# Optimization experiments

Hardware: AMD Instinct MI355X
Metric: run time of the kernel (lower is better)

The kernel has to match this reference:

```python
import jax, jax.numpy as jnp
import numpy as np

NB_KERNEL = 16
NUM_POS_EMB = 16
DMAX = 20.0


def _grbf_encode(d):
    # d: (..., ) distances; centers 0..DMAX in NB_KERNEL steps (matches torch.arange(0, 20*(1+1/15), 20/15))
    centers = jnp.linspace(0.0, DMAX, NB_KERNEL, dtype=jnp.float32)
    return jnp.exp(-jnp.square(d[..., None] - centers))


def _positional_embeddings(d):
    # d: (..., ) float offsets
    freq = jnp.exp(jnp.arange(0, NUM_POS_EMB, 2, dtype=jnp.float32) * (-(np.log(10000.0) / NUM_POS_EMB)))
    angles = d[..., None] * freq  # (..., NUM_POS_EMB//2)
    return jnp.concatenate([jnp.cos(angles), jnp.sin(angles)], axis=-1)


def setup_inputs() -> dict:
    key = jax.random.key(0)
    # coordinates in Angstrom-ish scale so pairwise distances span the RBF range
    crd = jax.random.normal(key, (4096, 4, 3), dtype=jnp.float32) * 10.0
    return {"crd": crd, "max_neigh": 64}


def reference(crd, max_neigh):
    nb_var = crd.shape[0]
    nb_neigh = min(max_neigh, nb_var - 1)

    # virtual Cbeta atom from backbone geometry
    b = crd[:, 1] - crd[:, 0]
    c = crd[:, 2] - crd[:, 1]
    a = jnp.cross(b, c)
    Cb = -0.58273431 * a + 0.56802827 * b - 0.54067466 * c + crd[:, 1]
    crd5 = jnp.concatenate([crd, Cb[:, None, :]], axis=1)  # (N, 5, 3)

    # pairwise CA distances, diagonal forced to -1 so self sorts first
    ca = crd5[:, 1]  # (N, 3)
    D = jnp.linalg.norm(ca[:, None, :] - ca[None, :, :], axis=-1)  # (N, N)
    diag = jnp.arange(nb_var)
    D = D.at[diag, diag].set(-1.0)

    # nb_neigh smallest distances (= top_k of -D); self is column 0
    neg_d, idx_pairs = jax.lax.top_k(-D, nb_neigh)  # (N, K)
    d = -neg_d
    d = d.at[:, 0].set(0.0)
    d = jnp.nan_to_num(d, nan=0.0)

    # all-pairs atom distances between residue i (5 atoms) and each neighbor j (5 atoms)
    neigh = crd5[idx_pairs]  # (N, K, 5, 3)
    diff = crd5[:, None, :, None, :] - neigh[:, :, None, :, :]  # (N, K, 5, 5, 3); [i,k,a,b]=crd[i,a]-crd[j,b]
    dist = jnp.linalg.norm(diff, axis=-1).reshape(nb_var, nb_neigh, 25)
    dist = _grbf_encode(dist).reshape(nb_var, nb_neigh, 25 * NB_KERNEL)
    dist = jnp.nan_to_num(dist, nan=0.0)

    # sinusoidal encoding of sequence-index offsets
    offsets = jnp.abs(diag[:, None] - idx_pairs).astype(jnp.float32)  # (N, K)
    pos = _positional_embeddings(offsets)  # (N, K, NUM_POS_EMB)

    return (d, dist, pos, idx_pairs)
```

## Files before the change

### kernel.cpp

```cpp
#include <hip/hip_runtime.h>
#include <math.h>

#define NBV 4096
#define KNE 64
#define D_OFF    0
#define DIST_OFF (NBV*KNE)
#define POS_OFF  (DIST_OFF + NBV*KNE*400)
#define IDX_OFF  (POS_OFF + NBV*KNE*16)

#define WS_CRD5 0
#define WS_CA4  (NBV*16)
#define WS_FLOATS (NBV*16 + NBV*4)

typedef float f4v __attribute__((ext_vector_type(4)));

__device__ __forceinline__ unsigned int f2sort(float f) {
  unsigned int u = __float_as_uint(f);
  return (u & 0x80000000u) ? ~u : (u | 0x80000000u);
}
__device__ __forceinline__ float sort2f(unsigned int s) {
  unsigned int u = (s & 0x80000000u) ? (s & 0x7FFFFFFFu) : ~s;
  return __uint_as_float(u);
}

__device__ __forceinline__ float4 crd5_f4(const float* __restrict__ crd, int r,
                                          int q) {
  if (q < 3) return ((const float4*)crd)[r * 3 + q];
  const float4 a = ((const float4*)crd)[r * 3 + 0];
  const float4 b = ((const float4*)crd)[r * 3 + 1];
  const float4 c = ((const float4*)crd)[r * 3 + 2];
  const float bx = a.w - a.x, by = b.x - a.y, bz = b.y - a.z;
  const float cx = b.z - a.w, cy = b.w - b.x, cz = c.x - b.y;
  const float axv = by * cz - bz * cy;
  const float ayv = bz * cx - bx * cz;
  const float azv = bx * cy - by * cx;
  return make_float4(
      -0.58273431f * axv + 0.56802827f * bx - 0.54067466f * cx + a.w,
      -0.58273431f * ayv + 0.56802827f * by - 0.54067466f * cy + b.x,
      -0.58273431f * azv + 0.56802827f * bz - 0.54067466f * cz + b.y, 0.0f);
}

__global__ __launch_bounds__(256) void prep_k(const float* __restrict__ crd,
                                              float* __restrict__ ws) {
  const int r = blockIdx.x * 256 + threadIdx.x;
  const float4 a = ((const float4*)crd)[r * 3 + 0];
  const float4 b = ((const float4*)crd)[r * 3 + 1];
  const float4 c = ((const float4*)crd)[r * 3 + 2];
  const float bx = a.w - a.x, by = b.x - a.y, bz = b.y - a.z;
  const float cx = b.z - a.w, cy = b.w - b.x, cz = c.x - b.y;
  const float axv = by * cz - bz * cy;
  const float ayv = bz * cx - bx * cz;
  const float azv = bx * cy - by * cx;
  const float cbx = -0.58273431f * axv + 0.56802827f * bx - 0.54067466f * cx + a.w;
  const float cby = -0.58273431f * ayv + 0.56802827f * by - 0.54067466f * cy + b.x;
  const float cbz = -0.58273431f * azv + 0.56802827f * bz - 0.54067466f * cz + b.y;

  float4* row = (float4*)(ws + WS_CRD5 + r * 16);
  row[0] = a;
  row[1] = b;
  row[2] = c;
  row[3] = make_float4(cbx, cby, cbz, 0.0f);
  ((float4*)(ws + WS_CA4))[r] = make_float4(a.w, b.x, b.y, 0.0f);
}

template <bool USE_WS>
__global__ __launch_bounds__(256) void fused_k(const float* __restrict__ crd,
                                               const float* __restrict__ ws,
                                               float* __restrict__ out) {
  const int i = blockIdx.x;
  const int t = threadIdx.x;

  __shared__ float region0[2688];
  __shared__ unsigned long long cand[512];
  __shared__ int jidx[64];
  __shared__ unsigned int cnt;
  __shared__ int selbin;
  __shared__ unsigned int wsum[4];

  unsigned int* hist = (unsigned int*)region0;
  float* rows = region0;
  float* dvals = region0 + 1040;

  for (int b = t; b < 2048; b += 256) hist[b] = 0u;
  if (t == 0) cnt = 0u;
  __syncthreads();

  float cax, cay, caz;
  if (USE_WS) {
    const float4 c4 = ((const float4*)(ws + WS_CA4))[i];
    cax = c4.x; cay = c4.y; caz = c4.z;
  } else {
    cax = crd[i * 12 + 3]; cay = crd[i * 12 + 4]; caz = crd[i * 12 + 5];
  }

  float dv[16];
#pragma unroll
  for (int s = 0; s < 16; s++) {
    const int j = t + 256 * s;
    float jx, jy, jz;
    if (USE_WS) {
      const float4 c4 = ((const float4*)(ws + WS_CA4))[j];
      jx = c4.x; jy = c4.y; jz = c4.z;
    } else {
      jx = crd[j * 12 + 3]; jy = crd[j * 12 + 4]; jz = crd[j * 12 + 5];
    }
    const float dx = cax - jx, dy = cay - jy, dz = caz - jz;
    float f = sqrtf(dx * dx + dy * dy + dz * dz);
    if (j == i) f = -1.0f;
    dv[s] = f;
    int b = (int)(f * 16.0f);
    b = b < 0 ? 0 : (b > 2047 ? 2047 : b);
    atomicAdd(&hist[b], 1u);
  }
  __syncthreads();

  unsigned int bc[8];
  unsigned int loc = 0;
#pragma unroll
  for (int r = 0; r < 8; r++) { bc[r] = hist[t * 8 + r]; loc += bc[r]; }
  const int lane = t & 63, wid = t >> 6;
  unsigned int x = loc;
#pragma unroll
  for (int off = 1; off < 64; off <<= 1) {
    unsigned int y = __shfl_up(x, off, 64);
    if (lane >= off) x += y;
  }
  if (lane == 63) wsum[wid] = x;
  __syncthreads();
  unsigned int woff = 0;
#pragma unroll
  for (int w = 0; w < 4; w++)
    if (w < wid) woff += wsum[w];
  unsigned int c = woff + x - loc;
#pragma unroll
  for (int r = 0; r < 8; r++) {
    if (c < 64u && c + bc[r] >= 64u) selbin = t * 8 + r;
    c += bc[r];
  }
  __syncthreads();
  const int B = selbin;

#pragma unroll
  for (int s = 0; s < 16; s++) {
    const float f = dv[s];
    int b = (int)(f * 16.0f);
    b = b < 0 ? 0 : (b > 2047 ? 2047 : b);
    if (b <= B) {
      const unsigned int p = atomicAdd(&cnt, 1u);
      if (p < 512u) {
        const int j = t + 256 * s;
        cand[p] = (((unsigned long long)f2sort(f)) << 32) | (unsigned int)j;
      }
    }
  }
  __syncthreads();
  unsigned int M = cnt;
  if (M > 512u) M = 512u;
  for (int p = t; p < 512; p += 256)
    if ((unsigned)p >= M) cand[p] = 0xFFFFFFFFFFFFFFFFull;

  int P = 64;
  while (P < (int)M) P <<= 1;
  for (int ksz = 2; ksz <= P; ksz <<= 1) {
    for (int jsz = ksz >> 1; jsz > 0; jsz >>= 1) {
      __syncthreads();
      if (t < (P >> 1)) {
        const int a = ((t & ~(jsz - 1)) << 1) | (t & (jsz - 1));
        const int b2 = a | jsz;
        const unsigned long long va = cand[a], vb = cand[b2];
        const bool up = ((a & ksz) == 0);
        if ((va > vb) == up) { cand[a] = vb; cand[b2] = va; }
      }
    }
  }
  __syncthreads();

  if (t < KNE) {
    const unsigned long long key = cand[t];
    const int j = (int)(unsigned int)(key & 0xFFFFFFFFull);
    const float f = sort2f((unsigned int)(key >> 32));
    jidx[t] = j;
    out[D_OFF + i * KNE + t] = (t == 0) ? 0.0f : f;
    out[IDX_OFF + i * KNE + t] = (float)j;
  }
  __syncthreads();

  const int sr = t >> 2, qq = t & 3;
  float4 v, v2;
  if (USE_WS) v = ((const float4*)ws)[jidx[sr] * 4 + qq];
  else        v = crd5_f4(crd, jidx[sr], qq);
  if (t < 4) {
    if (USE_WS) v2 = ((const float4*)ws)[i * 4 + t];
    else        v2 = crd5_f4(crd, i, t);
  }

  {
    const int n = sr, g = qq;
    const int j = jidx[n];
    int di = i - j;
    if (di < 0) di = -di;
    const float offv = (float)di;
    const bool hi = (g & 1);
    const float fA = hi ? 0.01f                   : 1.0f;
    const float fB = hi ? 0.0031622776601683794f  : 0.31622776601683794f;
    const float fC = hi ? 0.001f                  : 0.1f;
    const float fD = hi ? 0.00031622776601683794f : 0.031622776601683791f;
    float s0, c0, s1, c1, s2, c2, s3, c3;
    sincosf(offv * fA, &s0, &c0);
    sincosf(offv * fB, &s1, &c1);
    sincosf(offv * fC, &s2, &c2);
    sincosf(offv * fD, &s3, &c3);
    f4v o;
    if (g < 2) o = (f4v){c0, c1, c2, c3};
    else       o = (f4v){s0, s1, s2, s3};
    f4v* pv = (f4v*)(out + POS_OFF) + (size_t)(i * KNE + n) * 4 + g;
    __builtin_nontemporal_store(o, pv);
  }

  ((float4*)rows)[sr * 4 + qq] = v;
  if (t < 4) ((float4*)rows)[64 * 4 + t] = v2;
  __syncthreads();

#pragma unroll
  for (int it = 0; it < 7; it++) {
    const int pid = t + 256 * it;
    if (pid < 1600) {
      const int k = pid / 25;
      const int p = pid - k * 25;
      const int p0 = p / 5;
      const int p1 = p - p0 * 5;
      const float dx = rows[64 * 16 + p0 * 3 + 0] - rows[k * 16 + p1 * 3 + 0];
      const float dy = rows[64 * 16 + p0 * 3 + 1] - rows[k * 16 + p1 * 3 + 1];
      const float dz = rows[64 * 16 + p0 * 3 + 2] - rows[k * 16 + p1 * 3 + 2];
      dvals[pid] = sqrtf(dx * dx + dy * dy + dz * dz);
    }
  }
  __syncthreads();

  const float step = 20.0f / 15.0f;
  const float TWO_S = 2.6666667f;
  const float S2 = 1.7777778f;
  const float RHO = 0.02856550f;
  f4v* dst = (f4v*)(out + DIST_OFF) + (size_t)i * 6400;
#pragma unroll
  for (int s = 0; s < 25; s++) {
    const int f4i = t + 256 * s;
    const int pair = f4i >> 2;
    const float cb0 = (float)((f4i & 3) * 4) * step;
    float u = dvals[pair] - cb0;
    u = fminf(u, 16.0f);
    float e = __expf(-u * u);
    float q = __expf(fmaf(TWO_S, u, -S2));
    f4v o;
    o.x = e;
    e *= q;           o.y = e;
    q *= RHO; e *= q; o.z = e;
    q *= RHO; e *= q; o.w = e;
    __builtin_nontemporal_store(o, dst + f4i);
  }
}

extern "C" void kernel_launch(void* const* d_in, const int* in_sizes, int n_in,
                              void* d_out, int out_size, void* d_ws, size_t ws_size,
                              hipStream_t stream) {
  const float* crd = (const float*)d_in[0];
  float* out = (float*)d_out;
  if (ws_size >= (size_t)WS_FLOATS * sizeof(float)) {
    float* ws = (float*)d_ws;
    hipLaunchKernelGGL(prep_k, dim3(NBV / 256), dim3(256), 0, stream, crd, ws);
    hipLaunchKernelGGL(fused_k<true>, dim3(NBV), dim3(256), 0, stream, crd, ws,
                       out);
  } else {
    hipLaunchKernelGGL(fused_k<false>, dim3(NBV), dim3(256), 0, stream, crd,
                       (const float*)nullptr, out);
  }
}
```

Before: 448.1 us.

## Split fused kernel into neighbor-selection and RBF distance kernels via workspace

The single fused per-residue kernel is split into two launches. The first does histogram-based top-k selection, writes d, idx and positional embeddings, and stores the neighbor indices to workspace. The second reloads those indices and computes the 5x5 atom distances and RBF encoding with smaller shared memory. This lets each kernel run with its own register and LDS footprint so the store-heavy RBF phase can reach higher occupancy, at the cost of an extra launch and a small workspace round trip. The fallback fused path is kept, without workspace, for when the workspace is too small.

```diff
diff --git a/kernel.cpp b/kernel.cpp
--- a/kernel.cpp
+++ b/kernel.cpp
@@ -10,7 +10,8 @@
 
 #define WS_CRD5 0
 #define WS_CA4  (NBV*16)
-#define WS_FLOATS (NBV*16 + NBV*4)
+#define WS_JIDX (NBV*20)
+#define WS_FLOATS (NBV*20 + NBV*KNE)
 
 typedef float f4v __attribute__((ext_vector_type(4)));
 
@@ -63,48 +64,31 @@
   ((float4*)(ws + WS_CA4))[r] = make_float4(a.w, b.x, b.y, 0.0f);
 }
 
-template <bool USE_WS>
-__global__ __launch_bounds__(256) void fused_k(const float* __restrict__ crd,
-                                               const float* __restrict__ ws,
-                                               float* __restrict__ out) {
+__global__ __launch_bounds__(256) void selA_k(const float* __restrict__ ws,
+                                              float* __restrict__ out,
+                                              int* __restrict__ jidx_ws) {
   const int i = blockIdx.x;
   const int t = threadIdx.x;
 
-  __shared__ float region0[2688];
+  __shared__ unsigned int hist[2048];
   __shared__ unsigned long long cand[512];
   __shared__ int jidx[64];
   __shared__ unsigned int cnt;
   __shared__ int selbin;
   __shared__ unsigned int wsum[4];
 
-  unsigned int* hist = (unsigned int*)region0;
-  float* rows = region0;
-  float* dvals = region0 + 1040;
-
   for (int b = t; b < 2048; b += 256) hist[b] = 0u;
   if (t == 0) cnt = 0u;
   __syncthreads();
 
-  float cax, cay, caz;
-  if (USE_WS) {
-    const float4 c4 = ((const float4*)(ws + WS_CA4))[i];
-    cax = c4.x; cay = c4.y; caz = c4.z;
-  } else {
-    cax = crd[i * 12 + 3]; cay = crd[i * 12 + 4]; caz = crd[i * 12 + 5];
-  }
+  const float4 ci = ((const float4*)(ws + WS_CA4))[i];
 
   float dv[16];
 #pragma unroll
   for (int s = 0; s < 16; s++) {
     const int j = t + 256 * s;
-    float jx, jy, jz;
-    if (USE_WS) {
-      const float4 c4 = ((const float4*)(ws + WS_CA4))[j];
-      jx = c4.x; jy = c4.y; jz = c4.z;
-    } else {
-      jx = crd[j * 12 + 3]; jy = crd[j * 12 + 4]; jz = crd[j * 12 + 5];
-    }
-    const float dx = cax - jx, dy = cay - jy, dz = caz - jz;
+    const float4 cj = ((const float4*)(ws + WS_CA4))[j];
+    const float dx = ci.x - cj.x, dy = ci.y - cj.y, dz = ci.z - cj.z;
     float f = sqrtf(dx * dx + dy * dy + dz * dz);
     if (j == i) f = -1.0f;
     dv[s] = f;
@@ -180,19 +164,210 @@
     const int j = (int)(unsigned int)(key & 0xFFFFFFFFull);
     const float f = sort2f((unsigned int)(key >> 32));
     jidx[t] = j;
+    jidx_ws[i * KNE + t] = j;
     out[D_OFF + i * KNE + t] = (t == 0) ? 0.0f : f;
     out[IDX_OFF + i * KNE + t] = (float)j;
   }
   __syncthreads();
 
+  {
+    const int n = t >> 2, g = t & 3;
+    const int j = jidx[n];
+    int di = i - j;
+    if (di < 0) di = -di;
+    const float offv = (float)di;
+    const bool hi = (g & 1);
+    const float fA = hi ? 0.01f                   : 1.0f;
+    const float fB = hi ? 0.0031622776601683794f  : 0.31622776601683794f;
+    const float fC = hi ? 0.001f                  : 0.1f;
+    const float fD = hi ? 0.00031622776601683794f : 0.031622776601683791f;
+    float s0, c0, s1, c1, s2, c2, s3, c3;
+    sincosf(offv * fA, &s0, &c0);
+    sincosf(offv * fB, &s1, &c1);
+    sincosf(offv * fC, &s2, &c2);
+    sincosf(offv * fD, &s3, &c3);
+    f4v o;
+    if (g < 2) o = (f4v){c0, c1, c2, c3};
+    else       o = (f4v){s0, s1, s2, s3};
+    f4v* pv = (f4v*)(out + POS_OFF) + (size_t)(i * KNE + n) * 4 + g;
+    __builtin_nontemporal_store(o, pv);
+  }
+}
+
+__global__ __launch_bounds__(256) void distB_k(const float* __restrict__ ws,
+                                               const int* __restrict__ jidx_ws,
+                                               float* __restrict__ out) {
+  const int i = blockIdx.x;
+  const int t = threadIdx.x;
+
+  __shared__ float rows[65 * 16];
+  __shared__ float dvals[1600];
+  __shared__ int jidx[64];
+
+  if (t < 64) jidx[t] = jidx_ws[i * KNE + t];
+  __syncthreads();
+
+  {
+    const int sr = t >> 2, qq = t & 3;
+    ((float4*)rows)[sr * 4 + qq] = ((const float4*)ws)[jidx[sr] * 4 + qq];
+    if (t < 4) ((float4*)rows)[64 * 4 + t] = ((const float4*)ws)[i * 4 + t];
+  }
+  __syncthreads();
+
+#pragma unroll
+  for (int it = 0; it < 7; it++) {
+    const int pid = t + 256 * it;
+    if (pid < 1600) {
+      const int k = pid / 25;
+      const int p = pid - k * 25;
+      const int p0 = p / 5;
+      const int p1 = p - p0 * 5;
+      const float dx = rows[64 * 16 + p0 * 3 + 0] - rows[k * 16 + p1 * 3 + 0];
+      const float dy = rows[64 * 16 + p0 * 3 + 1] - rows[k * 16 + p1 * 3 + 1];
+      const float dz = rows[64 * 16 + p0 * 3 + 2] - rows[k * 16 + p1 * 3 + 2];
+      dvals[pid] = sqrtf(dx * dx + dy * dy + dz * dz);
+    }
+  }
+  __syncthreads();
+
+  const float step = 20.0f / 15.0f;
+  const float TWO_S = 2.6666667f;
+  const float S2 = 1.7777778f;
+  const float RHO = 0.02856550f;
+  f4v* dst = (f4v*)(out + DIST_OFF) + (size_t)i * 6400;
+#pragma unroll
+  for (int s = 0; s < 25; s++) {
+    const int f4i = t + 256 * s;
+    const int pair = f4i >> 2;
+    const float cb0 = (float)((f4i & 3) * 4) * step;
+    float u = dvals[pair] - cb0;
+    u = fminf(u, 16.0f);
+    float e = __expf(-u * u);
+    float q = __expf(fmaf(TWO_S, u, -S2));
+    f4v o;
+    o.x = e;
+    e *= q;           o.y = e;
+    q *= RHO; e *= q; o.z = e;
+    q *= RHO; e *= q; o.w = e;
+    __builtin_nontemporal_store(o, dst + f4i);
+  }
+}
+
+template <bool USE_WS>
+__global__ __launch_bounds__(256) void fused_k(const float* __restrict__ crd,
+                                               const float* __restrict__ ws,
+                                               float* __restrict__ out) {
+  const int i = blockIdx.x;
+  const int t = threadIdx.x;
+
+  __shared__ float region0[2688];
+  __shared__ unsigned long long cand[512];
+  __shared__ int jidx[64];
+  __shared__ unsigned int cnt;
+  __shared__ int selbin;
+  __shared__ unsigned int wsum[4];
+
+  unsigned int* hist = (unsigned int*)region0;
+  float* rows = region0;
+  float* dvals = region0 + 1040;
+
+  for (int b = t; b < 2048; b += 256) hist[b] = 0u;
+  if (t == 0) cnt = 0u;
+  __syncthreads();
+
+  float cax, cay, caz;
+  cax = crd[i * 12 + 3]; cay = crd[i * 12 + 4]; caz = crd[i * 12 + 5];
+
+  float dv[16];
+#pragma unroll
+  for (int s = 0; s < 16; s++) {
+    const int j = t + 256 * s;
+    float jx = crd[j * 12 + 3], jy = crd[j * 12 + 4], jz = crd[j * 12 + 5];
+    const float dx = cax - jx, dy = cay - jy, dz = caz - jz;
+    float f = sqrtf(dx * dx + dy * dy + dz * dz);
+    if (j == i) f = -1.0f;
+    dv[s] = f;
+    int b = (int)(f * 16.0f);
+    b = b < 0 ? 0 : (b > 2047 ? 2047 : b);
+    atomicAdd(&hist[b], 1u);
+  }
+  __syncthreads();
+
+  unsigned int bc[8];
+  unsigned int loc = 0;
+#pragma unroll
+  for (int r = 0; r < 8; r++) { bc[r] = hist[t * 8 + r]; loc += bc[r]; }
+  const int lane = t & 63, wid = t >> 6;
+  unsigned int x = loc;
+#pragma unroll
+  for (int off = 1; off < 64; off <<= 1) {
+    unsigned int y = __shfl_up(x, off, 64);
+    if (lane >= off) x += y;
+  }
+  if (lane == 63) wsum[wid] = x;
+  __syncthreads();
+  unsigned int woff = 0;
+#pragma unroll
+  for (int w = 0; w < 4; w++)
+    if (w < wid) woff += wsum[w];
+  unsigned int c = woff + x - loc;
+#pragma unroll
+  for (int r = 0; r < 8; r++) {
+    if (c < 64u && c + bc[r] >= 64u) selbin = t * 8 + r;
+    c += bc[r];
+  }
+  __syncthreads();
+  const int B = selbin;
+
+#pragma unroll
+  for (int s = 0; s < 16; s++) {
+    const float f = dv[s];
+    int b = (int)(f * 16.0f);
+    b = b < 0 ? 0 : (b > 2047 ? 2047 : b);
+    if (b <= B) {
+      const unsigned int p = atomicAdd(&cnt, 1u);
+      if (p < 512u) {
+        const int j = t + 256 * s;
+        cand[p] = (((unsigned long long)f2sort(f)) << 32) | (unsigned int)j;
+      }
+    }
+  }
+  __syncthreads();
+  unsigned int M = cnt;
+  if (M > 512u) M = 512u;
+  for (int p = t; p < 512; p += 256)
+    if ((unsigned)p >= M) cand[p] = 0xFFFFFFFFFFFFFFFFull;
+
+  int P = 64;
+  while (P < (int)M) P <<= 1;
+  for (int ksz = 2; ksz <= P; ksz <<= 1) {
+    for (int jsz = ksz >> 1; jsz > 0; jsz >>= 1) {
+      __syncthreads();
+      if (t < (P >> 1)) {
+        const int a = ((t & ~(jsz - 1)) << 1) | (t & (jsz - 1));
+        const int b2 = a | jsz;
+        const unsigned long long va = cand[a], vb = cand[b2];
+        const bool up = ((a & ksz) == 0);
+        if ((va > vb) == up) { cand[a] = vb; cand[b2] = va; }
+      }
+    }
+  }
+  __syncthreads();
+
+  if (t < KNE) {
+    const unsigned long long key = cand[t];
+    const int j = (int)(unsigned int)(key & 0xFFFFFFFFull);
+    const float f = sort2f((unsigned int)(key >> 32));
+    jidx[t] = j;
+    out[D_OFF + i * KNE + t] = (t == 0) ? 0.0f : f;
+    out[IDX_OFF + i * KNE + t] = (float)j;
+  }
+  __syncthreads();
+
   const int sr = t >> 2, qq = t & 3;
   float4 v, v2;
-  if (USE_WS) v = ((const float4*)ws)[jidx[sr] * 4 + qq];
-  else        v = crd5_f4(crd, jidx[sr], qq);
-  if (t < 4) {
-    if (USE_WS) v2 = ((const float4*)ws)[i * 4 + t];
-    else        v2 = crd5_f4(crd, i, t);
-  }
+  v = crd5_f4(crd, jidx[sr], qq);
+  if (t < 4) v2 = crd5_f4(crd, i, t);
 
   {
     const int n = sr, g = qq;
@@ -267,8 +442,11 @@
   float* out = (float*)d_out;
   if (ws_size >= (size_t)WS_FLOATS * sizeof(float)) {
     float* ws = (float*)d_ws;
+    int* jidx_ws = (int*)(ws + WS_JIDX);
     hipLaunchKernelGGL(prep_k, dim3(NBV / 256), dim3(256), 0, stream, crd, ws);
-    hipLaunchKernelGGL(fused_k<true>, dim3(NBV), dim3(256), 0, stream, crd, ws,
+    hipLaunchKernelGGL(selA_k, dim3(NBV), dim3(256), 0, stream, ws, out,
+                       jidx_ws);
+    hipLaunchKernelGGL(distB_k, dim3(NBV), dim3(256), 0, stream, ws, jidx_ws,
                        out);
   } else {
     hipLaunchKernelGGL(fused_k<false>, dim3(NBV), dim3(256), 0, stream, crd,
```

Result: slower. 472.6 us (+5.5%).

## Use wave-aggregated atomics and rank-by-counting instead of bitonic sort for top-k

Applied to the files above, without the earlier changes.

Candidate compaction now uses one atomicAdd per wavefront, with a ballot/popcount prefix replacing a per-thread LDS atomic. The bitonic sort over up to 512 candidates, which needed many block barriers, is replaced by a counting-rank selection. Each thread computes the rank of its candidates by scanning all M keys and writes only ranks below 64. This removes the barrier-heavy sort but adds O(M^2) LDS reads, which grows costly if many candidates fall into the selected bin.

```diff
diff --git a/kernel.cpp b/kernel.cpp
--- a/kernel.cpp
+++ b/kernel.cpp
@@ -140,13 +140,20 @@
   __syncthreads();
   const int B = selbin;
 
+  const unsigned long long lmask = (1ull << lane) - 1ull;
 #pragma unroll
   for (int s = 0; s < 16; s++) {
     const float f = dv[s];
     int b = (int)(f * 16.0f);
     b = b < 0 ? 0 : (b > 2047 ? 2047 : b);
-    if (b <= B) {
-      const unsigned int p = atomicAdd(&cnt, 1u);
+    const bool pred = (b <= B);
+    const unsigned long long mask = __ballot(pred);
+    unsigned int base = 0;
+    if (lane == 0 && mask)
+      base = atomicAdd(&cnt, (unsigned int)__popcll(mask));
+    base = __shfl(base, 0, 64);
+    if (pred) {
+      const unsigned int p = base + (unsigned int)__popcll(mask & lmask);
       if (p < 512u) {
         const int j = t + 256 * s;
         cand[p] = (((unsigned long long)f2sort(f)) << 32) | (unsigned int)j;
@@ -154,34 +161,22 @@
     }
   }
   __syncthreads();
-  unsigned int M = cnt;
-  if (M > 512u) M = 512u;
-  for (int p = t; p < 512; p += 256)
-    if ((unsigned)p >= M) cand[p] = 0xFFFFFFFFFFFFFFFFull;
-
-  int P = 64;
-  while (P < (int)M) P <<= 1;
-  for (int ksz = 2; ksz <= P; ksz <<= 1) {
-    for (int jsz = ksz >> 1; jsz > 0; jsz >>= 1) {
-      __syncthreads();
-      if (t < (P >> 1)) {
-        const int a = ((t & ~(jsz - 1)) << 1) | (t & (jsz - 1));
-        const int b2 = a | jsz;
-        const unsigned long long va = cand[a], vb = cand[b2];
-        const bool up = ((a & ksz) == 0);
-        if ((va > vb) == up) { cand[a] = vb; cand[b2] = va; }
+
+  {
+    unsigned int M = cnt;
+    if (M > 512u) M = 512u;
+    for (int p = t; p < (int)M; p += 256) {
+      const unsigned long long key = cand[p];
+      int r = 0;
+      for (int q = 0; q < (int)M; q++) r += (cand[q] < key);
+      if (r < KNE) {
+        const int j = (int)(unsigned int)(key & 0xFFFFFFFFull);
+        const float f = sort2f((unsigned int)(key >> 32));
+        jidx[r] = j;
+        out[D_OFF + i * KNE + r] = (r == 0) ? 0.0f : f;
+        out[IDX_OFF + i * KNE + r] = (float)j;
       }
     }
-  }
-  __syncthreads();
-
-  if (t < KNE) {
-    const unsigned long long key = cand[t];
-    const int j = (int)(unsigned int)(key & 0xFFFFFFFFull);
-    const float f = sort2f((unsigned int)(key >> 32));
-    jidx[t] = j;
-    out[D_OFF + i * KNE + t] = (t == 0) ? 0.0f : f;
-    out[IDX_OFF + i * KNE + t] = (float)j;
   }
   __syncthreads();
 
```

After: 445.4 us. Within noise of the previous version (-0.6%).
